# Kernel tuning notes

Measured on AMD Instinct MI355X. Metric: run time of the kernel, lower is better.

## Reference

```python
import jax, jax.numpy as jnp
import numpy as np

N_NODES = 100000
N_EDGES = 1000000
H = 128  # hidden_size


def setup_inputs() -> dict:
    key = jax.random.key(0)
    ks = jax.random.split(key, 8)
    emb = jax.random.normal(ks[0], (N_NODES, H), dtype=jnp.float32)
    edge_index = jax.random.randint(ks[1], (2, N_EDGES), 0, N_NODES, dtype=jnp.int64)
    # MLP([2H, 4H, H, 1]) weights (Kaiming-ish scaled normals)
    W1 = jax.random.normal(ks[2], (2 * H, 4 * H), dtype=jnp.float32) / np.sqrt(2 * H).astype(np.float32)
    b1 = jnp.zeros((4 * H,), dtype=jnp.float32)
    W2 = jax.random.normal(ks[3], (4 * H, H), dtype=jnp.float32) / np.sqrt(4 * H).astype(np.float32)
    b2 = jnp.zeros((H,), dtype=jnp.float32)
    W3 = jax.random.normal(ks[4], (H, 1), dtype=jnp.float32) / np.sqrt(H).astype(np.float32)
    b3 = jnp.zeros((1,), dtype=jnp.float32)
    return {"emb": emb, "edge_index": edge_index,
            "W1": W1, "b1": b1, "W2": W2, "b2": b2, "W3": W3, "b3": b3}


def reference(emb, edge_index, W1, b1, W2, b2, W3, b3):
    # ExtractorMLP.forward with learn_edge_att=True, eval mode.
    col = edge_index[0]
    row = edge_index[1]
    # edge-gather + concat: [E, 2H]
    f12 = jnp.concatenate([emb[col], emb[row]], axis=-1)
    # MLP([2H, 4H, H, 1]); Dropout is identity in eval mode
    h = jax.nn.relu(f12 @ W1 + b1)          # [E, 4H]
    h = jax.nn.relu(h @ W2 + b2)            # [E, H]
    att_log_logits = h @ W3 + b3            # [E, 1]
    # concrete_sample with training=False -> plain sigmoid
    att = jax.nn.sigmoid(att_log_logits)
    return att
```

## Files before the change

kernel.cpp:

```cpp
#include <hip/hip_runtime.h>
#include <math.h>

#define E_TOTAL   1000000
#define HDIM      128
#define K1        256
#define N1        512
#define N2        128
#define M_TILE    64
#define BLOCK     512

typedef _Float16 f16;
typedef _Float16 f16_4  __attribute__((ext_vector_type(4)));
typedef _Float16 f16_8  __attribute__((ext_vector_type(8)));
typedef float    f32_16 __attribute__((ext_vector_type(16)));

__global__ void prep_weights(const float* __restrict__ W1, const float* __restrict__ W2,
                             f16* __restrict__ W1F, f16* __restrict__ W2F) {
    int t = blockIdx.x * blockDim.x + threadIdx.x;
    const int total1 = K1 * N1;
    const int total2 = N1 * N2;
    if (t < total1) {
        int v    = t & 7;
        int lane = (t >> 3) & 63;
        int kc   = (t >> 9) & 15;
        int nt   = t >> 13;
        int k = kc * 16 + (lane >> 5) * 8 + v;
        int n = nt * 32 + (lane & 31);
        W1F[t] = (f16)W1[k * N1 + n];
    } else if (t < total1 + total2) {
        int u = t - total1;
        int v    = u & 7;
        int lane = (u >> 3) & 63;
        int kcg  = (u >> 9) & 31;
        int nt   = u >> 14;
        int k = kcg * 16 + (lane >> 5) * 8 + v;
        int n = nt * 32 + (lane & 31);
        W2F[u] = (f16)W2[k * N2 + n];
    }
}

__global__ void prep_emb(const float* __restrict__ emb, f16* __restrict__ emb16) {
    int t = blockIdx.x * blockDim.x + threadIdx.x;
    float4 f = ((const float4*)emb)[t];
    f16_4 v = { (f16)f.x, (f16)f.y, (f16)f.z, (f16)f.w };
    ((f16_4*)emb16)[t] = v;
}

template <bool F16EMB>
__global__ __launch_bounds__(BLOCK, 4) void edge_mlp_kernel(
    const float* __restrict__ emb,
    const f16*   __restrict__ emb16,
    const int*   __restrict__ eidx,
    const f16*   __restrict__ W1F,
    const float* __restrict__ b1,
    const f16*   __restrict__ W2F,
    const float* __restrict__ b2,
    const float* __restrict__ W3,
    const float* __restrict__ b3,
    float* __restrict__ out)
{
    __shared__ __align__(16) f16 sAF[2 * 16 * 64 * 8];
    __shared__ __align__(16) f16 sBF[2][2 * 8 * 64 * 8];
    f16* sH2F = sAF;

    const int tid = threadIdx.x;
    const int e0  = blockIdx.x * M_TILE;

    {
        const int m    = tid >> 3;
        const int side = (tid >> 2) & 1;
        const int sub  = tid & 3;
        const int met  = m >> 5;
        const int m31  = m & 31;
        const int node = eidx[side * E_TOTAL + e0 + m];
        if (F16EMB) {
            const f16* src = emb16 + (size_t)node * HDIM;
            #pragma unroll
            for (int j = 0; j < 2; ++j) {
                const int g = side * 8 + sub * 2 + j;
                const int koff = (sub * 2 + j) * 16;
                #pragma unroll
                for (int lh = 0; lh < 2; ++lh) {
                    f16_8 v = *(const f16_8*)(src + koff + lh * 8);
                    *(f16_8*)(sAF + (((met * 16 + g) * 64 + lh * 32 + m31) << 3)) = v;
                }
            }
        } else {
            const float* src = emb + (size_t)node * HDIM;
            #pragma unroll
            for (int j = 0; j < 2; ++j) {
                const int g = side * 8 + sub * 2 + j;
                const int koff = (sub * 2 + j) * 16;
                #pragma unroll
                for (int lh = 0; lh < 2; ++lh) {
                    float4 fa = *(const float4*)(src + koff + lh * 8);
                    float4 fb = *(const float4*)(src + koff + lh * 8 + 4);
                    f16_8 v = { (f16)fa.x, (f16)fa.y, (f16)fa.z, (f16)fa.w,
                                (f16)fb.x, (f16)fb.y, (f16)fb.z, (f16)fb.w };
                    *(f16_8*)(sAF + (((met * 16 + g) * 64 + lh * 32 + m31) << 3)) = v;
                }
            }
        }
    }
    __syncthreads();

    const int wv   = tid >> 6;
    const int lane = tid & 63;
    const int l31  = lane & 31;
    const int lh   = lane >> 5;
    const int et   = wv & 1;
    const int wnt  = wv >> 1;

    f32_16 acc2 = {0.f};

    {
        f32_16 acc1 = {0.f};
        const int nt = wnt;
        #pragma unroll
        for (int kc = 0; kc < 16; ++kc) {
            f16_8 ef = *(const f16_8*)(sAF + (((et * 16 + kc) * 64 + lane) << 3));
            f16_8 wf = *(const f16_8*)(W1F + (((nt * 16 + kc) * 64 + lane) << 3));
            acc1 = __builtin_amdgcn_mfma_f32_32x32x16_f16(wf, ef, acc1, 0, 0, 0);
        }
        f16* bcur = &sBF[0][0];
        #pragma unroll
        for (int g = 0; g < 4; ++g) {
            const int wnl = wnt * 32 + lh * 4 + g * 8;
            const float4 bv = *(const float4*)(b1 + wnl);
            f16_4 hv;
            #pragma unroll
            for (int i = 0; i < 4; ++i) {
                float v = acc1[g * 4 + i] + ((const float*)&bv)[i];
                hv[i] = (f16)(v > 0.f ? v : 0.f);
            }
            const int kl = wnt * 2 + (g >> 1);
            *(f16_4*)(bcur + ((((et * 8 + kl) * 64 + (g & 1) * 32 + l31) << 3) + lh * 4)) = hv;
        }
    }
    __syncthreads();

    #pragma unroll
    for (int q = 1; q < 4; ++q) {
        f32_16 acc1 = {0.f};
        const int nt = q * 4 + wnt;
        const f16* bprev = &sBF[(q - 1) & 1][0];
        #pragma unroll
        for (int kc = 0; kc < 16; ++kc) {
            f16_8 ef = *(const f16_8*)(sAF + (((et * 16 + kc) * 64 + lane) << 3));
            f16_8 wf = *(const f16_8*)(W1F + (((nt * 16 + kc) * 64 + lane) << 3));
            acc1 = __builtin_amdgcn_mfma_f32_32x32x16_f16(wf, ef, acc1, 0, 0, 0);
            if (kc < 8) {
                const int kcg = (q - 1) * 8 + kc;
                f16_8 ef2 = *(const f16_8*)(bprev + (((et * 8 + kc) * 64 + lane) << 3));
                f16_8 wf2 = *(const f16_8*)(W2F + (((wnt * 32 + kcg) * 64 + lane) << 3));
                acc2 = __builtin_amdgcn_mfma_f32_32x32x16_f16(wf2, ef2, acc2, 0, 0, 0);
            }
        }
        f16* bcur = &sBF[q & 1][0];
        #pragma unroll
        for (int g = 0; g < 4; ++g) {
            const int wnl = wnt * 32 + lh * 4 + g * 8;
            const float4 bv = *(const float4*)(b1 + q * 128 + wnl);
            f16_4 hv;
            #pragma unroll
            for (int i = 0; i < 4; ++i) {
                float v = acc1[g * 4 + i] + ((const float*)&bv)[i];
                hv[i] = (f16)(v > 0.f ? v : 0.f);
            }
            const int kl = wnt * 2 + (g >> 1);
            *(f16_4*)(bcur + ((((et * 8 + kl) * 64 + (g & 1) * 32 + l31) << 3) + lh * 4)) = hv;
        }
        __syncthreads();
    }

    {
        const f16* bprev = &sBF[1][0];
        #pragma unroll
        for (int kc = 0; kc < 8; ++kc) {
            const int kcg = 24 + kc;
            f16_8 ef2 = *(const f16_8*)(bprev + (((et * 8 + kc) * 64 + lane) << 3));
            f16_8 wf2 = *(const f16_8*)(W2F + (((wnt * 32 + kcg) * 64 + lane) << 3));
            acc2 = __builtin_amdgcn_mfma_f32_32x32x16_f16(wf2, ef2, acc2, 0, 0, 0);
        }
    }

    {
        #pragma unroll
        for (int g = 0; g < 4; ++g) {
            const int wn = wnt * 32 + lh * 4 + g * 8;
            const float4 bv = *(const float4*)(b2 + wn);
            f16_4 hv;
            #pragma unroll
            for (int i = 0; i < 4; ++i) {
                float v = acc2[g * 4 + i] + ((const float*)&bv)[i];
                hv[i] = (f16)(v > 0.f ? v : 0.f);
            }
            const int kl = wnt * 2 + (g >> 1);
            *(f16_4*)(sH2F + ((((et * 8 + kl) * 64 + (g & 1) * 32 + l31) << 3) + lh * 4)) = hv;
        }
    }
    __syncthreads();

    {
        const int m   = tid >> 3;
        const int j   = tid & 7;
        const int met = m >> 5;
        const int m31 = m & 31;
        f16_8 a = *(const f16_8*)(sH2F + (((met * 8 + j) * 64 + m31) << 3));
        f16_8 b = *(const f16_8*)(sH2F + (((met * 8 + j) * 64 + 32 + m31) << 3));
        const float4* w3v = (const float4*)(W3 + j * 16);
        float4 w0 = w3v[0], w1 = w3v[1], w2 = w3v[2], w3 = w3v[3];
        float s = 0.f;
        s += (float)a[0]*w0.x + (float)a[1]*w0.y + (float)a[2]*w0.z + (float)a[3]*w0.w;
        s += (float)a[4]*w1.x + (float)a[5]*w1.y + (float)a[6]*w1.z + (float)a[7]*w1.w;
        s += (float)b[0]*w2.x + (float)b[1]*w2.y + (float)b[2]*w2.z + (float)b[3]*w2.w;
        s += (float)b[4]*w3.x + (float)b[5]*w3.y + (float)b[6]*w3.z + (float)b[7]*w3.w;
        s += __shfl_xor(s, 1);
        s += __shfl_xor(s, 2);
        s += __shfl_xor(s, 4);
        if (j == 0) {
            const float logit = s + b3[0];
            out[e0 + m] = 1.0f / (1.0f + __expf(-logit));
        }
    }
}

extern "C" void kernel_launch(void* const* d_in, const int* in_sizes, int n_in,
                              void* d_out, int out_size, void* d_ws, size_t ws_size,
                              hipStream_t stream) {
    const float* emb  = (const float*)d_in[0];
    const int*   eidx = (const int*)d_in[1];
    const float* W1   = (const float*)d_in[2];
    const float* b1   = (const float*)d_in[3];
    const float* W2   = (const float*)d_in[4];
    const float* b2   = (const float*)d_in[5];
    const float* W3   = (const float*)d_in[6];
    const float* b3   = (const float*)d_in[7];
    float* out = (float*)d_out;

    const size_t wbytes   = (size_t)(K1 * N1 + N1 * N2) * sizeof(f16);
    const size_t embbytes = (size_t)100000 * HDIM * sizeof(f16);

    f16* W1F = (f16*)d_ws;
    f16* W2F = W1F + K1 * N1;

    const int prep_total = K1 * N1 + N1 * N2;
    prep_weights<<<(prep_total + 255) / 256, 256, 0, stream>>>(W1, W2, W1F, W2F);

    if (ws_size >= wbytes + embbytes) {
        f16* emb16 = W2F + N1 * N2;
        const int cvt_threads = 100000 * HDIM / 4;
        prep_emb<<<cvt_threads / 256, 256, 0, stream>>>(emb, emb16);
        edge_mlp_kernel<true><<<E_TOTAL / M_TILE, BLOCK, 0, stream>>>(
            emb, emb16, eidx, W1F, b1, W2F, b2, W3, b3, out);
    } else {
        edge_mlp_kernel<false><<<E_TOTAL / M_TILE, BLOCK, 0, stream>>>(
            emb, (const f16*)nullptr, eidx, W1F, b1, W2F, b2, W3, b3, out);
    }
}
```

Measured before the change: 616.4 us.

## Halve block to 4 waves, each covering both edge tiles for weight reuse

The block shrinks from 8 waves to 4. Each wave now computes both 32-edge sub-tiles against the same weight fragment, so every W1/W2 global load feeds two MFMAs instead of one. This halves weight-fragment traffic per block. In exchange each wave holds twice the accumulator registers and the launch-bounds occupancy hint drops from 4 to 2 blocks per CU, which may reduce latency hiding for the gather and weight loads.

```diff
diff --git a/kernel.cpp b/kernel.cpp
--- a/kernel.cpp
+++ b/kernel.cpp
@@ -7,7 +7,7 @@
 #define N1        512
 #define N2        128
 #define M_TILE    64
-#define BLOCK     512
+#define BLOCK     256
 
 typedef _Float16 f16;
 typedef _Float16 f16_4  __attribute__((ext_vector_type(4)));
@@ -47,7 +47,7 @@
 }
 
 template <bool F16EMB>
-__global__ __launch_bounds__(BLOCK, 4) void edge_mlp_kernel(
+__global__ __launch_bounds__(BLOCK, 2) void edge_mlp_kernel(
     const float* __restrict__ emb,
     const f16*   __restrict__ emb16,
     const int*   __restrict__ eidx,
@@ -67,18 +67,18 @@
     const int e0  = blockIdx.x * M_TILE;
 
     {
-        const int m    = tid >> 3;
-        const int side = (tid >> 2) & 1;
-        const int sub  = tid & 3;
+        const int m    = tid >> 2;
+        const int side = (tid >> 1) & 1;
+        const int sub  = tid & 1;
         const int met  = m >> 5;
         const int m31  = m & 31;
         const int node = eidx[side * E_TOTAL + e0 + m];
         if (F16EMB) {
             const f16* src = emb16 + (size_t)node * HDIM;
             #pragma unroll
-            for (int j = 0; j < 2; ++j) {
-                const int g = side * 8 + sub * 2 + j;
-                const int koff = (sub * 2 + j) * 16;
+            for (int j = 0; j < 4; ++j) {
+                const int g = side * 8 + sub * 4 + j;
+                const int koff = (sub * 4 + j) * 16;
                 #pragma unroll
                 for (int lh = 0; lh < 2; ++lh) {
                     f16_8 v = *(const f16_8*)(src + koff + lh * 8);
@@ -88,9 +88,9 @@
         } else {
             const float* src = emb + (size_t)node * HDIM;
             #pragma unroll
-            for (int j = 0; j < 2; ++j) {
-                const int g = side * 8 + sub * 2 + j;
-                const int koff = (sub * 2 + j) * 16;
+            for (int j = 0; j < 4; ++j) {
+                const int g = side * 8 + sub * 4 + j;
+                const int koff = (sub * 4 + j) * 16;
                 #pragma unroll
                 for (int lh = 0; lh < 2; ++lh) {
                     float4 fa = *(const float4*)(src + koff + lh * 8);
@@ -104,71 +104,84 @@
     }
     __syncthreads();
 
-    const int wv   = tid >> 6;
+    const int wnt  = tid >> 6;
     const int lane = tid & 63;
     const int l31  = lane & 31;
     const int lh   = lane >> 5;
-    const int et   = wv & 1;
-    const int wnt  = wv >> 1;
-
-    f32_16 acc2 = {0.f};
-
-    {
-        f32_16 acc1 = {0.f};
+
+    f32_16 acc2[2] = {{0.f}, {0.f}};
+
+    {
+        f32_16 acc1[2] = {{0.f}, {0.f}};
         const int nt = wnt;
         #pragma unroll
         for (int kc = 0; kc < 16; ++kc) {
-            f16_8 ef = *(const f16_8*)(sAF + (((et * 16 + kc) * 64 + lane) << 3));
             f16_8 wf = *(const f16_8*)(W1F + (((nt * 16 + kc) * 64 + lane) << 3));
-            acc1 = __builtin_amdgcn_mfma_f32_32x32x16_f16(wf, ef, acc1, 0, 0, 0);
+            #pragma unroll
+            for (int et = 0; et < 2; ++et) {
+                f16_8 ef = *(const f16_8*)(sAF + (((et * 16 + kc) * 64 + lane) << 3));
+                acc1[et] = __builtin_amdgcn_mfma_f32_32x32x16_f16(wf, ef, acc1[et], 0, 0, 0);
+            }
         }
         f16* bcur = &sBF[0][0];
         #pragma unroll
-        for (int g = 0; g < 4; ++g) {
-            const int wnl = wnt * 32 + lh * 4 + g * 8;
-            const float4 bv = *(const float4*)(b1 + wnl);
-            f16_4 hv;
-            #pragma unroll
-            for (int i = 0; i < 4; ++i) {
-                float v = acc1[g * 4 + i] + ((const float*)&bv)[i];
-                hv[i] = (f16)(v > 0.f ? v : 0.f);
-            }
-            const int kl = wnt * 2 + (g >> 1);
-            *(f16_4*)(bcur + ((((et * 8 + kl) * 64 + (g & 1) * 32 + l31) << 3) + lh * 4)) = hv;
+        for (int et = 0; et < 2; ++et) {
+            #pragma unroll
+            for (int g = 0; g < 4; ++g) {
+                const int wnl = wnt * 32 + lh * 4 + g * 8;
+                const float4 bv = *(const float4*)(b1 + wnl);
+                f16_4 hv;
+                #pragma unroll
+                for (int i = 0; i < 4; ++i) {
+                    float v = acc1[et][g * 4 + i] + ((const float*)&bv)[i];
+                    hv[i] = (f16)(v > 0.f ? v : 0.f);
+                }
+                const int kl = wnt * 2 + (g >> 1);
+                *(f16_4*)(bcur + ((((et * 8 + kl) * 64 + (g & 1) * 32 + l31) << 3) + lh * 4)) = hv;
+            }
         }
     }
     __syncthreads();
 
     #pragma unroll
     for (int q = 1; q < 4; ++q) {
-        f32_16 acc1 = {0.f};
+        f32_16 acc1[2] = {{0.f}, {0.f}};
         const int nt = q * 4 + wnt;
         const f16* bprev = &sBF[(q - 1) & 1][0];
         #pragma unroll
         for (int kc = 0; kc < 16; ++kc) {
-            f16_8 ef = *(const f16_8*)(sAF + (((et * 16 + kc) * 64 + lane) << 3));
             f16_8 wf = *(const f16_8*)(W1F + (((nt * 16 + kc) * 64 + lane) << 3));
-            acc1 = __builtin_amdgcn_mfma_f32_32x32x16_f16(wf, ef, acc1, 0, 0, 0);
+            #pragma unroll
+            for (int et = 0; et < 2; ++et) {
+                f16_8 ef = *(const f16_8*)(sAF + (((et * 16 + kc) * 64 + lane) << 3));
+                acc1[et] = __builtin_amdgcn_mfma_f32_32x32x16_f16(wf, ef, acc1[et], 0, 0, 0);
+            }
             if (kc < 8) {
                 const int kcg = (q - 1) * 8 + kc;
-                f16_8 ef2 = *(const f16_8*)(bprev + (((et * 8 + kc) * 64 + lane) << 3));
                 f16_8 wf2 = *(const f16_8*)(W2F + (((wnt * 32 + kcg) * 64 + lane) << 3));
-                acc2 = __builtin_amdgcn_mfma_f32_32x32x16_f16(wf2, ef2, acc2, 0, 0, 0);
+                #pragma unroll
+                for (int et = 0; et < 2; ++et) {
+                    f16_8 ef2 = *(const f16_8*)(bprev + (((et * 8 + kc) * 64 + lane) << 3));
+                    acc2[et] = __builtin_amdgcn_mfma_f32_32x32x16_f16(wf2, ef2, acc2[et], 0, 0, 0);
+                }
             }
         }
         f16* bcur = &sBF[q & 1][0];
         #pragma unroll
-        for (int g = 0; g < 4; ++g) {
-            const int wnl = wnt * 32 + lh * 4 + g * 8;
-            const float4 bv = *(const float4*)(b1 + q * 128 + wnl);
-            f16_4 hv;
-            #pragma unroll
-            for (int i = 0; i < 4; ++i) {
-                float v = acc1[g * 4 + i] + ((const float*)&bv)[i];
-                hv[i] = (f16)(v > 0.f ? v : 0.f);
-            }
-            const int kl = wnt * 2 + (g >> 1);
-            *(f16_4*)(bcur + ((((et * 8 + kl) * 64 + (g & 1) * 32 + l31) << 3) + lh * 4)) = hv;
+        for (int et = 0; et < 2; ++et) {
+            #pragma unroll
+            for (int g = 0; g < 4; ++g) {
+                const int wnl = wnt * 32 + lh * 4 + g * 8;
+                const float4 bv = *(const float4*)(b1 + q * 128 + wnl);
+                f16_4 hv;
+                #pragma unroll
+                for (int i = 0; i < 4; ++i) {
+                    float v = acc1[et][g * 4 + i] + ((const float*)&bv)[i];
+                    hv[i] = (f16)(v > 0.f ? v : 0.f);
+                }
+                const int kl = wnt * 2 + (g >> 1);
+                *(f16_4*)(bcur + ((((et * 8 + kl) * 64 + (g & 1) * 32 + l31) << 3) + lh * 4)) = hv;
+            }
         }
         __syncthreads();
     }
@@ -178,46 +191,55 @@
         #pragma unroll
         for (int kc = 0; kc < 8; ++kc) {
             const int kcg = 24 + kc;
-            f16_8 ef2 = *(const f16_8*)(bprev + (((et * 8 + kc) * 64 + lane) << 3));
             f16_8 wf2 = *(const f16_8*)(W2F + (((wnt * 32 + kcg) * 64 + lane) << 3));
-            acc2 = __builtin_amdgcn_mfma_f32_32x32x16_f16(wf2, ef2, acc2, 0, 0, 0);
-        }
-    }
-
-    {
-        #pragma unroll
-        for (int g = 0; g < 4; ++g) {
-            const int wn = wnt * 32 + lh * 4 + g * 8;
-            const float4 bv = *(const float4*)(b2 + wn);
-            f16_4 hv;
-            #pragma unroll
-            for (int i = 0; i < 4; ++i) {
-                float v = acc2[g * 4 + i] + ((const float*)&bv)[i];
-                hv[i] = (f16)(v > 0.f ? v : 0.f);
-            }
-            const int kl = wnt * 2 + (g >> 1);
-            *(f16_4*)(sH2F + ((((et * 8 + kl) * 64 + (g & 1) * 32 + l31) << 3) + lh * 4)) = hv;
+            #pragma unroll
+            for (int et = 0; et < 2; ++et) {
+                f16_8 ef2 = *(const f16_8*)(bprev + (((et * 8 + kc) * 64 + lane) << 3));
+                acc2[et] = __builtin_amdgcn_mfma_f32_32x32x16_f16(wf2, ef2, acc2[et], 0, 0, 0);
+            }
+        }
+    }
+
+    {
+        #pragma unroll
+        for (int et = 0; et < 2; ++et) {
+            #pragma unroll
+            for (int g = 0; g < 4; ++g) {
+                const int wn = wnt * 32 + lh * 4 + g * 8;
+                const float4 bv = *(const float4*)(b2 + wn);
+                f16_4 hv;
+                #pragma unroll
+                for (int i = 0; i < 4; ++i) {
+                    float v = acc2[et][g * 4 + i] + ((const float*)&bv)[i];
+                    hv[i] = (f16)(v > 0.f ? v : 0.f);
+                }
+                const int kl = wnt * 2 + (g >> 1);
+                *(f16_4*)(sH2F + ((((et * 8 + kl) * 64 + (g & 1) * 32 + l31) << 3) + lh * 4)) = hv;
+            }
         }
     }
     __syncthreads();
 
     {
-        const int m   = tid >> 3;
-        const int j   = tid & 7;
+        const int m   = tid >> 2;
+        const int j   = tid & 3;
         const int met = m >> 5;
         const int m31 = m & 31;
-        f16_8 a = *(const f16_8*)(sH2F + (((met * 8 + j) * 64 + m31) << 3));
-        f16_8 b = *(const f16_8*)(sH2F + (((met * 8 + j) * 64 + 32 + m31) << 3));
-        const float4* w3v = (const float4*)(W3 + j * 16);
-        float4 w0 = w3v[0], w1 = w3v[1], w2 = w3v[2], w3 = w3v[3];
         float s = 0.f;
-        s += (float)a[0]*w0.x + (float)a[1]*w0.y + (float)a[2]*w0.z + (float)a[3]*w0.w;
-        s += (float)a[4]*w1.x + (float)a[5]*w1.y + (float)a[6]*w1.z + (float)a[7]*w1.w;
-        s += (float)b[0]*w2.x + (float)b[1]*w2.y + (float)b[2]*w2.z + (float)b[3]*w2.w;
-        s += (float)b[4]*w3.x + (float)b[5]*w3.y + (float)b[6]*w3.z + (float)b[7]*w3.w;
+        #pragma unroll
+        for (int jj = 0; jj < 2; ++jj) {
+            const int kl = j * 2 + jj;
+            f16_8 a = *(const f16_8*)(sH2F + (((met * 8 + kl) * 64 + m31) << 3));
+            f16_8 b = *(const f16_8*)(sH2F + (((met * 8 + kl) * 64 + 32 + m31) << 3));
+            const float4* w3v = (const float4*)(W3 + kl * 16);
+            float4 w0 = w3v[0], w1 = w3v[1], w2 = w3v[2], w3q = w3v[3];
+            s += (float)a[0]*w0.x + (float)a[1]*w0.y + (float)a[2]*w0.z + (float)a[3]*w0.w;
+            s += (float)a[4]*w1.x + (float)a[5]*w1.y + (float)a[6]*w1.z + (float)a[7]*w1.w;
+            s += (float)b[0]*w2.x + (float)b[1]*w2.y + (float)b[2]*w2.z + (float)b[3]*w2.w;
+            s += (float)b[4]*w3q.x + (float)b[5]*w3q.y + (float)b[6]*w3q.z + (float)b[7]*w3q.w;
+        }
         s += __shfl_xor(s, 1);
         s += __shfl_xor(s, 2);
-        s += __shfl_xor(s, 4);
         if (j == 0) {
             const float logit = s + b3[0];
             out[e0 + m] = 1.0f / (1.0f + __expf(-logit));
```

Result: faster. 559.5 us (-9.2%).
